# Performance work log

Hardware: AMD Instinct MI355X
Metric: run time of the kernel (lower is better)

Reference implementation:

```python
import jax, jax.numpy as jnp
import numpy as np

EPS = 1e-6

def _l2norm(x, axis=-1):
    # F.normalize with eps=1e-12 clamp on the norm
    n = jnp.sqrt(jnp.sum(x * x, axis=axis, keepdims=True))
    return x / jnp.maximum(n, 1e-12)

def setup_inputs() -> dict:
    key = jax.random.key(0)
    k1, k2, k3, k4 = jax.random.split(key, 4)
    B, D = 512, 512
    mu1 = jax.random.normal(k1, (B, D), dtype=jnp.float32)
    mu2 = jax.random.normal(k2, (B, D), dtype=jnp.float32)
    sigma1_sq = jax.random.uniform(k3, (B, D), dtype=jnp.float32)
    sigma2_sq = jax.random.uniform(k4, (B, D), dtype=jnp.float32)
    logit_scale = jnp.float32(100.0)  # CLIP-style exp(t)
    return {"mu1": mu1, "sigma1_sq": sigma1_sq, "mu2": mu2,
            "sigma2_sq": sigma2_sq, "logit_scale": logit_scale}

def _bd_similarity(mu1, sigma1_sq, mu2, sigma2_sq):
    # Bhattacharyya-distance-based similarity matrix [B, B]
    n1 = _l2norm(mu1)
    n2 = _l2norm(mu2)
    B, D = n1.shape
    sigma_avg = 0.5 * (sigma1_sq[:, None, :] + sigma2_sq[None, :, :])  # [B,B,D]
    diff = n1[:, None, :] - n2[None, :, :]                              # [B,B,D]
    term1 = jnp.sum(diff * diff / (sigma_avg + EPS), axis=2)            # [B,B]
    log_det_avg = jnp.sum(jnp.log(sigma_avg + EPS), axis=2)             # [B,B]
    log_det1 = jnp.sum(jnp.log(sigma1_sq + EPS), axis=1)[:, None]       # [B,1]
    log_det2 = jnp.sum(jnp.log(sigma2_sq + EPS), axis=1)[None, :]       # [1,B]
    term2 = log_det_avg - 0.5 * (log_det1 + log_det2)
    bd = 0.125 * term1 + 0.5 * term2
    return jnp.exp(-bd / D)

def _confident_loss(mu1, sigma1_sq, mu2, sigma2_sq):
    n1 = _l2norm(mu1)
    n2 = _l2norm(mu2)
    B = n1.shape[0]
    # ||n1_i - n2_j||^2 via Gram expansion (no BxBxD intermediate)
    sq1 = jnp.sum(n1 * n1, axis=1)[:, None]
    sq2 = jnp.sum(n2 * n2, axis=1)[None, :]
    d2 = sq1 + sq2 - 2.0 * (n1 @ n2.T)                                  # [B,B]
    sim = jnp.exp(-d2)
    diag = jnp.diagonal(sim)                                            # [B]
    # topk k=1 over off-diagonal == row max with diagonal masked out
    neg_inf = jnp.asarray(-jnp.inf, sim.dtype)
    off = jnp.where(jnp.eye(B, dtype=bool), neg_inf, sim)
    neg_max = jnp.max(off, axis=1)                                      # [B]
    uncertainty = jnp.exp(-diag / neg_max)                              # [B]
    avg_sigma = 0.5 * (jnp.mean(sigma1_sq, axis=1) + jnp.mean(sigma2_sq, axis=1))
    var_loss = jnp.mean(uncertainty)
    u_n = _l2norm(uncertainty, axis=-1)
    s_n = _l2norm(avg_sigma, axis=-1)
    cos_sim = jnp.sum(u_n * s_n)  # both already unit vectors
    return 1.0 - cos_sim, var_loss * 0.5

def _cross_entropy_diag(logits):
    # mean CE with labels = arange(B): -log_softmax(logits)[i, i]
    return -jnp.mean(jnp.diagonal(jax.nn.log_softmax(logits, axis=1)))

def reference(mu1, sigma1_sq, mu2, sigma2_sq, logit_scale):
    sim = _bd_similarity(mu1, sigma1_sq, mu2, sigma2_sq)
    logits = logit_scale * sim
    loss_pro = 0.5 * (_cross_entropy_diag(logits) + _cross_entropy_diag(logits.T))
    loss_rank, var_loss = _confident_loss(mu1, sigma1_sq, mu2, sigma2_sq)
    return loss_pro, loss_rank * 2.4, var_loss
```

## Files before the change

kernel.cpp:

```cpp
#include <hip/hip_runtime.h>
#include <math.h>

#define BDIM 512
#define DDIM 512

constexpr float EPS   = 1e-6f;
constexpr float HEPS  = 0.5e-6f;
constexpr float LN2   = 0.6931471805599453f;
constexpr float LOG2E = 1.4426950408889634f;

__device__ __forceinline__ float wave_reduce_sum(float v) {
  #pragma unroll
  for (int o = 32; o > 0; o >>= 1) v += __shfl_down(v, o, 64);
  return v;
}
__device__ __forceinline__ float wave_reduce_max(float v) {
  #pragma unroll
  for (int o = 32; o > 0; o >>= 1) v = fmaxf(v, __shfl_down(v, o, 64));
  return v;
}

__global__ __launch_bounds__(256) void prep_kernel(
    const float* __restrict__ mu1, const float* __restrict__ s1,
    const float* __restrict__ mu2, const float* __restrict__ s2,
    float* __restrict__ nA, float* __restrict__ sA,
    float* __restrict__ nB, float* __restrict__ sB,
    float* __restrict__ ld,
    float* __restrict__ mrow) {
  const int r = blockIdx.x;
  const int which = blockIdx.y;
  const float* __restrict__ mu = which ? mu2 : mu1;
  const float* __restrict__ sg = which ? s2 : s1;
  float* __restrict__ nout = which ? nB : nA;
  float* __restrict__ sout = which ? sB : sA;
  const int t = threadIdx.x;

  const float a  = mu[r * DDIM + t];
  const float b  = mu[r * DDIM + t + 256];
  const float sa = sg[r * DDIM + t];
  const float sb = sg[r * DDIM + t + 256];

  float v0 = a * a + b * b;
  float v1 = __log2f(sa + EPS) + __log2f(sb + EPS);
  float v2 = sa + sb;

  __shared__ float red[3][4];
  __shared__ float sinv;
  const int wid = t >> 6, lane = t & 63;
  v0 = wave_reduce_sum(v0);
  v1 = wave_reduce_sum(v1);
  v2 = wave_reduce_sum(v2);
  if (lane == 0) { red[0][wid] = v0; red[1][wid] = v1; red[2][wid] = v2; }
  __syncthreads();
  if (t == 0) {
    float sq = red[0][0] + red[0][1] + red[0][2] + red[0][3];
    float lg = red[1][0] + red[1][1] + red[1][2] + red[1][3];
    float sm = red[2][0] + red[2][1] + red[2][2] + red[2][3];
    ld[which * BDIM + r]   = LN2 * lg;
    mrow[which * BDIM + r] = sm * (1.0f / DDIM);
    sinv = 1.0f / fmaxf(sqrtf(sq), 1e-12f);
  }
  __syncthreads();
  const float inv = sinv;
  nout[r * DDIM + t]       = a * inv;
  nout[r * DDIM + t + 256] = b * inv;
  sout[r * DDIM + t]       = fmaf(0.5f, sa, HEPS);
  sout[r * DDIM + t + 256] = fmaf(0.5f, sb, HEPS);
}

__global__ __launch_bounds__(256) void bd_kernel(
    const float* __restrict__ nA, const float* __restrict__ sA,
    const float* __restrict__ nB, const float* __restrict__ sB,
    float* __restrict__ t1p, float* __restrict__ ldap,
    float* __restrict__ dacp) {
  __shared__ __align__(16) float4 lds[4 * 64 * 17];

  const int t  = threadIdx.x;
  const int i0 = blockIdx.y * 64, j0 = blockIdx.x * 64;
  const int z  = blockIdx.z;
  const int ti = t >> 4;
  const int tj = t & 15;

  #pragma unroll
  for (int q = 0; q < 4; ++q) {
    const int rem = q * 256 + t, row = rem >> 4, dc = rem & 15;
    lds[0 * 1088 + row * 17 + dc] =
        *(const float4*)&nA[(i0 + row) * DDIM + z * 64 + dc * 4];
  }
  #pragma unroll
  for (int q = 0; q < 4; ++q) {
    const int rem = q * 256 + t, row = rem >> 4, dc = rem & 15;
    lds[1 * 1088 + row * 17 + dc] =
        *(const float4*)&sA[(i0 + row) * DDIM + z * 64 + dc * 4];
  }
  #pragma unroll
  for (int q = 0; q < 4; ++q) {
    const int rem = q * 256 + t, row = rem >> 4, dc = rem & 15;
    lds[2 * 1088 + row * 17 + dc] =
        *(const float4*)&nB[(j0 + row) * DDIM + z * 64 + dc * 4];
  }
  #pragma unroll
  for (int q = 0; q < 4; ++q) {
    const int rem = q * 256 + t, row = rem >> 4, dc = rem & 15;
    lds[3 * 1088 + row * 17 + dc] =
        *(const float4*)&sB[(j0 + row) * DDIM + z * 64 + dc * 4];
  }
  __syncthreads();

  float t1[4][4]  = {};
  float lda[4][4] = {};
  float dac[4][4] = {};

  const float4* __restrict__ pAn = lds + 0 * 1088 + ti * 17;
  const float4* __restrict__ pAs = lds + 1 * 1088 + ti * 17;
  const float4* __restrict__ pBn = lds + 2 * 1088 + tj * 17;
  const float4* __restrict__ pBs = lds + 3 * 1088 + tj * 17;

  for (int g2 = 0; g2 < 8; ++g2) {
    float m[4][4] = {{1.f,1.f,1.f,1.f},{1.f,1.f,1.f,1.f},
                     {1.f,1.f,1.f,1.f},{1.f,1.f,1.f,1.f}};
    #pragma unroll
    for (int h = 0; h < 2; ++h) {
      const int dc = g2 * 2 + h;
      float4 Bn[4], Bs[4];
      #pragma unroll
      for (int q = 0; q < 4; ++q) Bn[q] = pBn[q * 272 + dc];
      #pragma unroll
      for (int q = 0; q < 4; ++q) Bs[q] = pBs[q * 272 + dc];
      #pragma unroll
      for (int qi = 0; qi < 4; ++qi) {
        const float4 An = pAn[qi * 272 + dc];
        const float4 As = pAs[qi * 272 + dc];
        #pragma unroll
        for (int p2 = 0; p2 < 2; ++p2) {
          const float an0 = ((const float*)&An)[2 * p2];
          const float an1 = ((const float*)&An)[2 * p2 + 1];
          const float as0 = ((const float*)&As)[2 * p2];
          const float as1 = ((const float*)&As)[2 * p2 + 1];
          #pragma unroll
          for (int qj = 0; qj < 4; ++qj) {
            const float bn0 = ((const float*)&Bn[qj])[2 * p2];
            const float bn1 = ((const float*)&Bn[qj])[2 * p2 + 1];
            const float bs0 = ((const float*)&Bs[qj])[2 * p2];
            const float bs1 = ((const float*)&Bs[qj])[2 * p2 + 1];
            const float sv0 = as0 + bs0;
            const float sv1 = as1 + bs1;
            const float svp = sv0 * sv1;
            const float df0 = an0 - bn0;
            const float df1 = an1 - bn1;
            float num = (df0 * df0) * sv1;
            num = fmaf(df1 * df1, sv0, num);
            t1[qi][qj]  = fmaf(num, __builtin_amdgcn_rcpf(svp), t1[qi][qj]);
            m[qi][qj]  *= svp;
            dac[qi][qj] = fmaf(an0, bn0, dac[qi][qj]);
            dac[qi][qj] = fmaf(an1, bn1, dac[qi][qj]);
          }
        }
      }
    }
    #pragma unroll
    for (int qi = 0; qi < 4; ++qi)
      #pragma unroll
      for (int qj = 0; qj < 4; ++qj)
        lda[qi][qj] += __log2f(m[qi][qj]);
  }

  const size_t zb = (size_t)z * BDIM * BDIM;
  #pragma unroll
  for (int qi = 0; qi < 4; ++qi) {
    #pragma unroll
    for (int qj = 0; qj < 4; ++qj) {
      const size_t o = zb + (size_t)(i0 + 16 * qi + ti) * BDIM
                          + j0 + 16 * qj + tj;
      t1p[o]  = t1[qi][qj];
      ldap[o] = lda[qi][qj];
      dacp[o] = dac[qi][qj];
    }
  }
}

__global__ __launch_bounds__(256) void combine_kernel(
    const float* __restrict__ t1p, const float* __restrict__ ldap,
    const float* __restrict__ dacp, const float* __restrict__ ld,
    const float* __restrict__ lscale,
    float* __restrict__ sim, float* __restrict__ pmaxf,
    float* __restrict__ pdiag, float* __restrict__ lse_row,
    float* __restrict__ dlog) {
  const int i = blockIdx.x;
  const int t = threadIdx.x;
  const float l1 = ld[i];
  const float sc = *lscale;
  float rmax = 0.f;
  float lg[2];
  #pragma unroll
  for (int q = 0; q < 2; ++q) {
    const int j = t + q * 256;
    const size_t o = (size_t)i * BDIM + j;
    float t1 = 0.f, lda = 0.f, dac = 0.f;
    #pragma unroll
    for (int zz = 0; zz < 8; ++zz) {
      const size_t idx = (size_t)zz * BDIM * BDIM + o;
      t1 += t1p[idx]; lda += ldap[idx]; dac += dacp[idx];
    }
    const float bd = fmaf(0.125f, t1,
                          0.5f * (LN2 * lda - 0.5f * (l1 + ld[BDIM + j])));
    const float sv = exp2f(bd * (-LOG2E / (float)DDIM));
    sim[o] = sv;
    lg[q] = sc * sv;
    const float p = exp2f((2.0f * LOG2E) * dac);
    if (j == i) { pdiag[i] = p; dlog[i] = sc * sv; }
    else        rmax = fmaxf(rmax, p);
  }
  __shared__ float red[4];
  const int wid = t >> 6, lane = t & 63;

  float wm = wave_reduce_max(rmax);
  if (lane == 0) red[wid] = wm;
  __syncthreads();
  if (t == 0) pmaxf[i] = fmaxf(fmaxf(red[0], red[1]), fmaxf(red[2], red[3]));
  __syncthreads();

  float rm = wave_reduce_max(fmaxf(lg[0], lg[1]));
  if (lane == 0) red[wid] = rm;
  __syncthreads();
  rm = fmaxf(fmaxf(red[0], red[1]), fmaxf(red[2], red[3]));
  __syncthreads();
  float rs = wave_reduce_sum(exp2f((lg[0] - rm) * LOG2E) +
                             exp2f((lg[1] - rm) * LOG2E));
  if (lane == 0) red[wid] = rs;
  __syncthreads();
  if (t == 0)
    lse_row[i] = rm + LN2 * __log2f(red[0] + red[1] + red[2] + red[3]);
}

__global__ __launch_bounds__(256) void lse_col_kernel(
    const float* __restrict__ sim, const float* __restrict__ lscale,
    float* __restrict__ lse_col) {
  const int b = blockIdx.x;
  const int t = threadIdx.x;
  const float sc = *lscale;
  const float c0 = sc * sim[t * BDIM + b];
  const float c1 = sc * sim[(t + 256) * BDIM + b];

  __shared__ float red[4];
  const int wid = t >> 6, lane = t & 63;

  float cm = wave_reduce_max(fmaxf(c0, c1));
  if (lane == 0) red[wid] = cm;
  __syncthreads();
  cm = fmaxf(fmaxf(red[0], red[1]), fmaxf(red[2], red[3]));
  __syncthreads();

  float cs = wave_reduce_sum(exp2f((c0 - cm) * LOG2E) + exp2f((c1 - cm) * LOG2E));
  if (lane == 0) red[wid] = cs;
  __syncthreads();
  if (t == 0)
    lse_col[b] = cm + LN2 * __log2f(red[0] + red[1] + red[2] + red[3]);
}

__global__ __launch_bounds__(512) void final_kernel(
    const float* __restrict__ pdiag, const float* __restrict__ pmaxf,
    const float* __restrict__ mrow, const float* __restrict__ lse_row,
    const float* __restrict__ lse_col, const float* __restrict__ dlog,
    float* __restrict__ out) {
  const int t = threadIdx.x;
  const float pm = pmaxf[t];
  const float u  = exp2f(-(pdiag[t] / pm) * LOG2E);
  const float as = 0.5f * (mrow[t] + mrow[BDIM + t]);

  float vals[6];
  vals[0] = u;
  vals[1] = u * u;
  vals[2] = as * as;
  vals[3] = u * as;
  vals[4] = lse_row[t] - dlog[t];
  vals[5] = lse_col[t] - dlog[t];

  __shared__ float red[6][8];
  const int wid = t >> 6, lane = t & 63;
  #pragma unroll
  for (int k = 0; k < 6; ++k) {
    const float v = wave_reduce_sum(vals[k]);
    if (lane == 0) red[k][wid] = v;
  }
  __syncthreads();
  if (t == 0) {
    float s[6];
    #pragma unroll
    for (int k = 0; k < 6; ++k) {
      float a = 0.f;
      #pragma unroll
      for (int w = 0; w < 8; ++w) a += red[k][w];
      s[k] = a;
    }
    const float mean_u = s[0] * (1.0f / BDIM);
    const float cosv = s[3] / fmaxf(sqrtf(s[1]) * sqrtf(s[2]), 1e-24f);
    out[0] = 0.5f * (s[4] + s[5]) * (1.0f / BDIM);
    out[1] = 2.4f * (1.0f - cosv);
    out[2] = 0.5f * mean_u;
  }
}

extern "C" void kernel_launch(void* const* d_in, const int* in_sizes, int n_in,
                              void* d_out, int out_size, void* d_ws, size_t ws_size,
                              hipStream_t stream) {
  const float* mu1 = (const float*)d_in[0];
  const float* s1  = (const float*)d_in[1];
  const float* mu2 = (const float*)d_in[2];
  const float* s2  = (const float*)d_in[3];
  const float* lsc = (const float*)d_in[4];
  float* out = (float*)d_out;

  float* ws      = (float*)d_ws;
  float* nA      = ws;
  float* sA      = nA + BDIM * DDIM;
  float* nB      = sA + BDIM * DDIM;
  float* sB      = nB + BDIM * DDIM;
  float* sim     = sB + BDIM * DDIM;
  float* t1p     = sim + BDIM * BDIM;
  float* ldap    = t1p + 8 * BDIM * BDIM;
  float* dacp    = ldap + 8 * BDIM * BDIM;
  float* ld      = dacp + 8 * BDIM * BDIM;
  float* mrow    = ld + 2 * BDIM;
  float* pmaxf   = mrow + 2 * BDIM;
  float* pdiag   = pmaxf + BDIM;
  float* lse_row = pdiag + BDIM;
  float* lse_col = lse_row + BDIM;
  float* dlog    = lse_col + BDIM;

  prep_kernel<<<dim3(BDIM, 2), 256, 0, stream>>>(mu1, s1, mu2, s2, nA, sA,
                                                 nB, sB, ld, mrow);
  bd_kernel<<<dim3(8, 8, 8), 256, 0, stream>>>(nA, sA, nB, sB, t1p, ldap,
                                               dacp);
  combine_kernel<<<BDIM, 256, 0, stream>>>(t1p, ldap, dacp, ld, lsc, sim,
                                           pmaxf, pdiag, lse_row, dlog);
  lse_col_kernel<<<BDIM, 256, 0, stream>>>(sim, lsc, lse_col);
  final_kernel<<<1, 512, 0, stream>>>(pdiag, pmaxf, mrow, lse_row, lse_col,
                                      dlog, out);
}
```

Before: 53.91 us.

## Use fixed logsumexp shift and coalesced column sums; pack dot products as float2

Since sim lies in (0,1], logits are at most the scale, so the softmax max is replaced by the constant scale and exp(sc*(sim-1)) is stored once. This removes the max-reduction passes and lets the column logsumexp become a coalesced partial column-sum kernel, followed by a final reduction, instead of a strided per-column kernel. The bd inner loop also uses 2-wide vector FMAs for the dot-product accumulator, which may map to packed FP32 instructions. The fixed shift relies on sim being at most 1, which exp(-bd/D) guarantees if bd is non-negative; a very large scale could underflow the sums.

```diff
diff --git a/kernel.cpp b/kernel.cpp
--- a/kernel.cpp
+++ b/kernel.cpp
@@ -8,6 +8,8 @@
 constexpr float HEPS  = 0.5e-6f;
 constexpr float LN2   = 0.6931471805599453f;
 constexpr float LOG2E = 1.4426950408889634f;
+
+typedef float v2f __attribute__((ext_vector_type(2)));
 
 __device__ __forceinline__ float wave_reduce_sum(float v) {
   #pragma unroll
@@ -109,7 +111,7 @@
 
   float t1[4][4]  = {};
   float lda[4][4] = {};
-  float dac[4][4] = {};
+  v2f   dac2[4][4] = {};
 
   const float4* __restrict__ pAn = lds + 0 * 1088 + ti * 17;
   const float4* __restrict__ pAs = lds + 1 * 1088 + ti * 17;
@@ -131,29 +133,25 @@
       for (int qi = 0; qi < 4; ++qi) {
         const float4 An = pAn[qi * 272 + dc];
         const float4 As = pAs[qi * 272 + dc];
+        const v2f* an2 = (const v2f*)&An;
+        const v2f* as2 = (const v2f*)&As;
         #pragma unroll
         for (int p2 = 0; p2 < 2; ++p2) {
-          const float an0 = ((const float*)&An)[2 * p2];
-          const float an1 = ((const float*)&An)[2 * p2 + 1];
-          const float as0 = ((const float*)&As)[2 * p2];
-          const float as1 = ((const float*)&As)[2 * p2 + 1];
+          const v2f an = an2[p2];
+          const v2f as = as2[p2];
           #pragma unroll
           for (int qj = 0; qj < 4; ++qj) {
-            const float bn0 = ((const float*)&Bn[qj])[2 * p2];
-            const float bn1 = ((const float*)&Bn[qj])[2 * p2 + 1];
-            const float bs0 = ((const float*)&Bs[qj])[2 * p2];
-            const float bs1 = ((const float*)&Bs[qj])[2 * p2 + 1];
-            const float sv0 = as0 + bs0;
-            const float sv1 = as1 + bs1;
-            const float svp = sv0 * sv1;
-            const float df0 = an0 - bn0;
-            const float df1 = an1 - bn1;
-            float num = (df0 * df0) * sv1;
-            num = fmaf(df1 * df1, sv0, num);
-            t1[qi][qj]  = fmaf(num, __builtin_amdgcn_rcpf(svp), t1[qi][qj]);
-            m[qi][qj]  *= svp;
-            dac[qi][qj] = fmaf(an0, bn0, dac[qi][qj]);
-            dac[qi][qj] = fmaf(an1, bn1, dac[qi][qj]);
+            const v2f bn = ((const v2f*)&Bn[qj])[p2];
+            const v2f bs = ((const v2f*)&Bs[qj])[p2];
+            const v2f sv = as + bs;
+            const v2f df = an - bn;
+            const v2f d2 = df * df;
+            dac2[qi][qj] = __builtin_elementwise_fma(an, bn, dac2[qi][qj]);
+            float num = d2.x * sv.y;
+            num = fmaf(d2.y, sv.x, num);
+            const float svp = sv.x * sv.y;
+            t1[qi][qj] = fmaf(num, __builtin_amdgcn_rcpf(svp), t1[qi][qj]);
+            m[qi][qj] *= svp;
           }
         }
       }
@@ -174,7 +172,7 @@
                           + j0 + 16 * qj + tj;
       t1p[o]  = t1[qi][qj];
       ldap[o] = lda[qi][qj];
-      dacp[o] = dac[qi][qj];
+      dacp[o] = dac2[qi][qj].x + dac2[qi][qj].y;
     }
   }
 }
@@ -183,7 +181,7 @@
     const float* __restrict__ t1p, const float* __restrict__ ldap,
     const float* __restrict__ dacp, const float* __restrict__ ld,
     const float* __restrict__ lscale,
-    float* __restrict__ sim, float* __restrict__ pmaxf,
+    float* __restrict__ E, float* __restrict__ pmaxf,
     float* __restrict__ pdiag, float* __restrict__ lse_row,
     float* __restrict__ dlog) {
   const int i = blockIdx.x;
@@ -191,7 +189,7 @@
   const float l1 = ld[i];
   const float sc = *lscale;
   float rmax = 0.f;
-  float lg[2];
+  float esum = 0.f;
   #pragma unroll
   for (int q = 0; q < 2; ++q) {
     const int j = t + q * 256;
@@ -205,8 +203,9 @@
     const float bd = fmaf(0.125f, t1,
                           0.5f * (LN2 * lda - 0.5f * (l1 + ld[BDIM + j])));
     const float sv = exp2f(bd * (-LOG2E / (float)DDIM));
-    sim[o] = sv;
-    lg[q] = sc * sv;
+    const float e  = exp2f(sc * (sv - 1.0f) * LOG2E);
+    E[o] = e;
+    esum += e;
     const float p = exp2f((2.0f * LOG2E) * dac);
     if (j == i) { pdiag[i] = p; dlog[i] = sc * sv; }
     else        rmax = fmaxf(rmax, p);
@@ -220,50 +219,40 @@
   if (t == 0) pmaxf[i] = fmaxf(fmaxf(red[0], red[1]), fmaxf(red[2], red[3]));
   __syncthreads();
 
-  float rm = wave_reduce_max(fmaxf(lg[0], lg[1]));
-  if (lane == 0) red[wid] = rm;
-  __syncthreads();
-  rm = fmaxf(fmaxf(red[0], red[1]), fmaxf(red[2], red[3]));
-  __syncthreads();
-  float rs = wave_reduce_sum(exp2f((lg[0] - rm) * LOG2E) +
-                             exp2f((lg[1] - rm) * LOG2E));
+  float rs = wave_reduce_sum(esum);
   if (lane == 0) red[wid] = rs;
   __syncthreads();
   if (t == 0)
-    lse_row[i] = rm + LN2 * __log2f(red[0] + red[1] + red[2] + red[3]);
-}
-
-__global__ __launch_bounds__(256) void lse_col_kernel(
-    const float* __restrict__ sim, const float* __restrict__ lscale,
-    float* __restrict__ lse_col) {
-  const int b = blockIdx.x;
+    lse_row[i] = sc + LN2 * __log2f(red[0] + red[1] + red[2] + red[3]);
+}
+
+__global__ __launch_bounds__(256) void colsum_kernel(
+    const float* __restrict__ E, float* __restrict__ colpart) {
+  const int k = blockIdx.x;
   const int t = threadIdx.x;
-  const float sc = *lscale;
-  const float c0 = sc * sim[t * BDIM + b];
-  const float c1 = sc * sim[(t + 256) * BDIM + b];
-
-  __shared__ float red[4];
-  const int wid = t >> 6, lane = t & 63;
-
-  float cm = wave_reduce_max(fmaxf(c0, c1));
-  if (lane == 0) red[wid] = cm;
-  __syncthreads();
-  cm = fmaxf(fmaxf(red[0], red[1]), fmaxf(red[2], red[3]));
-  __syncthreads();
-
-  float cs = wave_reduce_sum(exp2f((c0 - cm) * LOG2E) + exp2f((c1 - cm) * LOG2E));
-  if (lane == 0) red[wid] = cs;
-  __syncthreads();
-  if (t == 0)
-    lse_col[b] = cm + LN2 * __log2f(red[0] + red[1] + red[2] + red[3]);
+  float a0 = 0.f, a1 = 0.f;
+  #pragma unroll 4
+  for (int r = 0; r < 32; ++r) {
+    const int row = k * 32 + r;
+    a0 += E[row * BDIM + t];
+    a1 += E[row * BDIM + t + 256];
+  }
+  colpart[k * BDIM + t]       = a0;
+  colpart[k * BDIM + t + 256] = a1;
 }
 
 __global__ __launch_bounds__(512) void final_kernel(
     const float* __restrict__ pdiag, const float* __restrict__ pmaxf,
     const float* __restrict__ mrow, const float* __restrict__ lse_row,
-    const float* __restrict__ lse_col, const float* __restrict__ dlog,
-    float* __restrict__ out) {
+    const float* __restrict__ colpart, const float* __restrict__ dlog,
+    const float* __restrict__ lscale, float* __restrict__ out) {
   const int t = threadIdx.x;
+  const float sc = *lscale;
+  float cs = 0.f;
+  #pragma unroll
+  for (int k = 0; k < 16; ++k) cs += colpart[k * BDIM + t];
+  const float lse_col = sc + LN2 * __log2f(cs);
+
   const float pm = pmaxf[t];
   const float u  = exp2f(-(pdiag[t] / pm) * LOG2E);
   const float as = 0.5f * (mrow[t] + mrow[BDIM + t]);
@@ -274,7 +263,7 @@
   vals[2] = as * as;
   vals[3] = u * as;
   vals[4] = lse_row[t] - dlog[t];
-  vals[5] = lse_col[t] - dlog[t];
+  vals[5] = lse_col - dlog[t];
 
   __shared__ float red[6][8];
   const int wid = t >> 6, lane = t & 63;
@@ -316,8 +305,8 @@
   float* sA      = nA + BDIM * DDIM;
   float* nB      = sA + BDIM * DDIM;
   float* sB      = nB + BDIM * DDIM;
-  float* sim     = sB + BDIM * DDIM;
-  float* t1p     = sim + BDIM * BDIM;
+  float* E       = sB + BDIM * DDIM;
+  float* t1p     = E + BDIM * BDIM;
   float* ldap    = t1p + 8 * BDIM * BDIM;
   float* dacp    = ldap + 8 * BDIM * BDIM;
   float* ld      = dacp + 8 * BDIM * BDIM;
@@ -325,16 +314,16 @@
   float* pmaxf   = mrow + 2 * BDIM;
   float* pdiag   = pmaxf + BDIM;
   float* lse_row = pdiag + BDIM;
-  float* lse_col = lse_row + BDIM;
-  float* dlog    = lse_col + BDIM;
+  float* dlog    = lse_row + BDIM;
+  float* colpart = dlog + BDIM;
 
   prep_kernel<<<dim3(BDIM, 2), 256, 0, stream>>>(mu1, s1, mu2, s2, nA, sA,
                                                  nB, sB, ld, mrow);
   bd_kernel<<<dim3(8, 8, 8), 256, 0, stream>>>(nA, sA, nB, sB, t1p, ldap,
                                                dacp);
-  combine_kernel<<<BDIM, 256, 0, stream>>>(t1p, ldap, dacp, ld, lsc, sim,
+  combine_kernel<<<BDIM, 256, 0, stream>>>(t1p, ldap, dacp, ld, lsc, E,
                                            pmaxf, pdiag, lse_row, dlog);
-  lse_col_kernel<<<BDIM, 256, 0, stream>>>(sim, lsc, lse_col);
-  final_kernel<<<1, 512, 0, stream>>>(pdiag, pmaxf, mrow, lse_row, lse_col,
-                                      dlog, out);
-}
+  colsum_kernel<<<16, 256, 0, stream>>>(E, colpart);
+  final_kernel<<<1, 512, 0, stream>>>(pdiag, pmaxf, mrow, lse_row, colpart,
+                                      dlog, lsc, out);
+}
```

Measured after the change: 66.79 us. 23.9% more time.
